# Optimization experiments

Measured on AMD Instinct MI355X. Metric: run time of the kernel, lower is better.

The kernel has to match this reference:

```python
import jax, jax.numpy as jnp
import numpy as np

B, IN, OUT = 8192, 4096, 2048  # OUT must equal 32*64 per betta/gamma sizes


def setup_inputs() -> dict:
    key = jax.random.key(0)
    kx, kw = jax.random.split(key, 2)
    X = jax.random.normal(kx, (B, IN), dtype=jnp.float32)
    # xavier-uniform-like init for W
    limit = float(np.sqrt(6.0 / (IN + OUT)))
    W = jax.random.uniform(kw, (IN, OUT), minval=-limit, maxval=limit, dtype=jnp.float32)
    absmean = jnp.abs(W).mean(axis=0)
    alpha = jnp.abs(W).mean()          # scalar, >= 0
    betta = absmean[:32]               # (32,), >= 0
    gamma = absmean[32:96]             # (64,), >= 0
    return {"X": X, "W": W, "alpha": alpha, "betta": betta, "gamma": gamma}


def reference(X, W, alpha, betta, gamma):
    # module applies relu_ to alpha/betta/gamma data before the functional call
    alpha = jax.nn.relu(alpha)
    betta = jax.nn.relu(betta)
    gamma = jax.nn.relu(gamma)
    X_bin = jnp.sign(X)                # (B, IN)
    W_bin = jnp.sign(W)                # (IN, OUT)
    # scale[i*64+j] = alpha * betta[i] * gamma[j] -> (OUT,)
    scale = (alpha * jnp.outer(betta, gamma)).reshape(-1)
    return (X_bin @ W_bin) * scale     # (B, OUT)
```

## Files before the change

### kernel.cpp

```cpp
#include <hip/hip_runtime.h>


#define M_DIM 8192
#define K_DIM 4096
#define N_DIM 2048
#define KB    (K_DIM / 2)

typedef int i32x4 __attribute__((ext_vector_type(4)));
typedef int i32x8 __attribute__((ext_vector_type(8)));
typedef float f32x16 __attribute__((ext_vector_type(16)));

__device__ __forceinline__ unsigned int nib4(float x) {
  unsigned int s = (__float_as_uint(x) >> 28) & 0x8u;
  return x == 0.0f ? 0u : (0x2u | s);
}

__device__ __forceinline__ void gload_lds16(const void* g, void* lds) {
  __builtin_amdgcn_global_load_lds(
      (const __attribute__((address_space(1))) unsigned int*)g,
      (__attribute__((address_space(3))) unsigned int*)lds, 16, 0, 0);
}

__global__ void binX4_kernel(const float* __restrict__ X,
                             unsigned int* __restrict__ Xq, int n16) {
  int stride = gridDim.x * blockDim.x;
  for (int i = blockIdx.x * blockDim.x + threadIdx.x; i < n16; i += stride) {
    size_t base = (size_t)i * 16;
    unsigned int lo = 0, hi = 0;
#pragma unroll
    for (int j = 0; j < 2; ++j) {
      float4 v0 = *(const float4*)&X[base + j * 8];
      float4 v1 = *(const float4*)&X[base + j * 8 + 4];
      unsigned int p = 0;
      p |= nib4(v0.x) << 0;  p |= nib4(v0.y) << 4;
      p |= nib4(v0.z) << 8;  p |= nib4(v0.w) << 12;
      p |= nib4(v1.x) << 16; p |= nib4(v1.y) << 20;
      p |= nib4(v1.z) << 24; p |= nib4(v1.w) << 28;
      if (j == 0) lo = p; else hi = p;
    }
    uint2 r; r.x = lo; r.y = hi;
    *(uint2*)&Xq[(size_t)i * 2] = r;
  }
}

__global__ void binW4_kernel(const float* __restrict__ W,
                             unsigned short* __restrict__ Wq) {
  __shared__ float tile[32][33];
  const int n0 = blockIdx.x * 32;
  const int k0 = blockIdx.y * 32;
  const int t = threadIdx.x;
  const int tc = t & 31;
  const int tr = t >> 5;
#pragma unroll
  for (int i = 0; i < 32; i += 8)
    tile[tr + i][tc] = W[(size_t)(k0 + tr + i) * N_DIM + n0 + tc];
  __syncthreads();
  const int r = t >> 3;
  const int c = t & 7;
  unsigned int b0 = nib4(tile[c * 4 + 0][r]) | (nib4(tile[c * 4 + 1][r]) << 4);
  unsigned int b1 = nib4(tile[c * 4 + 2][r]) | (nib4(tile[c * 4 + 3][r]) << 4);
  Wq[(size_t)(n0 + r) * (KB / 2) + (k0 >> 2) + c] = (unsigned short)(b0 | (b1 << 8));
}

__global__ __launch_bounds__(256) void gemm_fp4_kernel(
    const unsigned char* __restrict__ Aq,
    const unsigned char* __restrict__ Bq,
    const float* __restrict__ alpha,
    const float* __restrict__ betta,
    const float* __restrict__ gamma,
    float* __restrict__ C) {
  __shared__ __align__(16) unsigned char sA[128 * 128];
  __shared__ __align__(16) unsigned char sB[128 * 128];

  const int t = threadIdx.x;
  const int lane = t & 63;
  const int l31 = lane & 31;
  const int lhi = lane >> 5;
  const int w = t >> 6;
  const int wr = w >> 1, wc = w & 1;

  const int bid = blockIdx.x;
  const int bm = bid >> 4;
  const int bn = bid & 15;
  const int row0 = bm * 128;
  const int col0 = bn * 128;

  f32x16 acc[2][2];
#pragma unroll
  for (int m = 0; m < 2; ++m)
#pragma unroll
    for (int n = 0; n < 2; ++n)
#pragma unroll
      for (int r = 0; r < 16; ++r) acc[m][n][r] = 0.f;

  for (int ktb = 0; ktb < KB; ktb += 128) {
#pragma unroll
    for (int j = 0; j < 4; ++j) {
      int c = j * 256 + t;
      int r = c >> 3;
      int gg = (c & 7) ^ (r & 7);
      gload_lds16(&Aq[(size_t)(row0 + r) * KB + ktb + gg * 16], &sA[c * 16]);
      gload_lds16(&Bq[(size_t)(col0 + r) * KB + ktb + gg * 16], &sB[c * 16]);
    }
    __syncthreads();

#pragma unroll
    for (int kk = 0; kk < 4; ++kk) {
      const int g = kk * 2 + lhi;
      i32x8 av[2], bv[2];
#pragma unroll
      for (int fm = 0; fm < 2; ++fm) {
        const int rr = wr * 64 + fm * 32 + l31;
        i32x4 v = *(const i32x4*)&sA[rr * 128 + ((g ^ (rr & 7)) * 16)];
        av[fm][0] = v[0]; av[fm][1] = v[1]; av[fm][2] = v[2]; av[fm][3] = v[3];
        av[fm][4] = 0; av[fm][5] = 0; av[fm][6] = 0; av[fm][7] = 0;
      }
#pragma unroll
      for (int fn = 0; fn < 2; ++fn) {
        const int rr = wc * 64 + fn * 32 + l31;
        i32x4 v = *(const i32x4*)&sB[rr * 128 + ((g ^ (rr & 7)) * 16)];
        bv[fn][0] = v[0]; bv[fn][1] = v[1]; bv[fn][2] = v[2]; bv[fn][3] = v[3];
        bv[fn][4] = 0; bv[fn][5] = 0; bv[fn][6] = 0; bv[fn][7] = 0;
      }
#pragma unroll
      for (int fm = 0; fm < 2; ++fm)
#pragma unroll
        for (int fn = 0; fn < 2; ++fn)
          acc[fm][fn] = __builtin_amdgcn_mfma_scale_f32_32x32x64_f8f6f4(
              av[fm], bv[fn], acc[fm][fn], 4, 4,
              0, 0x7F7F7F7F, 0, 0x7F7F7F7F);
    }
    __syncthreads();
  }

  const float ra = fmaxf(alpha[0], 0.0f);
#pragma unroll
  for (int fn = 0; fn < 2; ++fn) {
    const int col = col0 + wc * 64 + fn * 32 + l31;
    const float sc = ra * fmaxf(betta[col >> 6], 0.0f) * fmaxf(gamma[col & 63], 0.0f);
#pragma unroll
    for (int fm = 0; fm < 2; ++fm) {
      const int rbase = row0 + wr * 64 + fm * 32 + 4 * lhi;
#pragma unroll
      for (int r = 0; r < 16; ++r) {
        const int row = rbase + (r & 3) + 8 * (r >> 2);
        C[(size_t)row * N_DIM + col] = acc[fm][fn][r] * sc;
      }
    }
  }
}

extern "C" void kernel_launch(void* const* d_in, const int* in_sizes, int n_in,
                              void* d_out, int out_size, void* d_ws, size_t ws_size,
                              hipStream_t stream) {
  const float* X = (const float*)d_in[0];
  const float* W = (const float*)d_in[1];
  const float* alpha = (const float*)d_in[2];
  const float* betta = (const float*)d_in[3];
  const float* gamma = (const float*)d_in[4];
  float* out = (float*)d_out;

  unsigned char* Xq = (unsigned char*)d_ws;
  unsigned char* Wq = Xq + (size_t)M_DIM * KB;

  binX4_kernel<<<2048, 256, 0, stream>>>(X, (unsigned int*)Xq,
                                         (M_DIM * K_DIM) / 16);
  binW4_kernel<<<dim3(N_DIM / 32, K_DIM / 32), 256, 0, stream>>>(
      W, (unsigned short*)Wq);
  gemm_fp4_kernel<<<(M_DIM / 128) * (N_DIM / 128), 256, 0, stream>>>(
      Xq, Wq, alpha, betta, gamma, out);
}
```

Before: 80.00 us.

## Double-buffer LDS with 256x256 tiles, 512 threads and block swizzle

```diff
diff --git a/kernel.cpp b/kernel.cpp
--- a/kernel.cpp
+++ b/kernel.cpp
@@ -5,6 +5,7 @@
 #define K_DIM 4096
 #define N_DIM 2048
 #define KB    (K_DIM / 2)
+#define NT    (K_DIM / 256)
 
 typedef int i32x4 __attribute__((ext_vector_type(4)));
 typedef int i32x8 __attribute__((ext_vector_type(8)));
@@ -19,6 +20,13 @@
   __builtin_amdgcn_global_load_lds(
       (const __attribute__((address_space(1))) unsigned int*)g,
       (__attribute__((address_space(3))) unsigned int*)lds, 16, 0, 0);
+}
+
+__device__ __forceinline__ i32x8 pad8(i32x4 v) {
+  i32x8 r;
+  r[0] = v[0]; r[1] = v[1]; r[2] = v[2]; r[3] = v[3];
+  r[4] = 0; r[5] = 0; r[6] = 0; r[7] = 0;
+  return r;
 }
 
 __global__ void binX4_kernel(const float* __restrict__ X,
@@ -62,75 +70,100 @@
   Wq[(size_t)(n0 + r) * (KB / 2) + (k0 >> 2) + c] = (unsigned short)(b0 | (b1 << 8));
 }
 
-__global__ __launch_bounds__(256) void gemm_fp4_kernel(
+__device__ __forceinline__ void stage_tile(const unsigned char* __restrict__ src,
+                                           unsigned char* lds, int t) {
+#pragma unroll
+  for (int p = 0; p < 4; ++p) {
+    int c = p * 512 + t;
+    int r = c >> 3;
+    int gg = (c & 7) ^ (r & 7);
+    gload_lds16(src + (size_t)r * KB + gg * 16, lds + c * 16);
+  }
+}
+
+__global__ __launch_bounds__(512, 2) void gemm_fp4_kernel(
     const unsigned char* __restrict__ Aq,
     const unsigned char* __restrict__ Bq,
     const float* __restrict__ alpha,
     const float* __restrict__ betta,
     const float* __restrict__ gamma,
     float* __restrict__ C) {
-  __shared__ __align__(16) unsigned char sA[128 * 128];
-  __shared__ __align__(16) unsigned char sB[128 * 128];
+  __shared__ __align__(16) unsigned char smem[131072];
 
   const int t = threadIdx.x;
   const int lane = t & 63;
   const int l31 = lane & 31;
   const int lhi = lane >> 5;
   const int w = t >> 6;
-  const int wr = w >> 1, wc = w & 1;
+  const int wr = w >> 2;
+  const int wc = w & 3;
 
   const int bid = blockIdx.x;
-  const int bm = bid >> 4;
-  const int bn = bid & 15;
-  const int row0 = bm * 128;
-  const int col0 = bn * 128;
-
-  f32x16 acc[2][2];
-#pragma unroll
-  for (int m = 0; m < 2; ++m)
-#pragma unroll
-    for (int n = 0; n < 2; ++n)
-#pragma unroll
-      for (int r = 0; r < 16; ++r) acc[m][n][r] = 0.f;
-
-  for (int ktb = 0; ktb < KB; ktb += 128) {
-#pragma unroll
-    for (int j = 0; j < 4; ++j) {
-      int c = j * 256 + t;
-      int r = c >> 3;
-      int gg = (c & 7) ^ (r & 7);
-      gload_lds16(&Aq[(size_t)(row0 + r) * KB + ktb + gg * 16], &sA[c * 16]);
-      gload_lds16(&Bq[(size_t)(col0 + r) * KB + ktb + gg * 16], &sB[c * 16]);
-    }
-    __syncthreads();
+  const int swz = (bid & 7) * 32 + (bid >> 3);
+  const int bn = swz >> 5;
+  const int bm = swz & 31;
+  const int row0 = bm * 256;
+  const int col0 = bn * 256;
+
+  const unsigned char* Asrc = Aq + (size_t)row0 * KB;
+  const unsigned char* Bsrc = Bq + (size_t)col0 * KB;
+
+  f32x16 acc[4][2];
+#pragma unroll
+  for (int fm = 0; fm < 4; ++fm)
+#pragma unroll
+    for (int fn = 0; fn < 2; ++fn)
+#pragma unroll
+      for (int r = 0; r < 16; ++r) acc[fm][fn][r] = 0.f;
+
+  stage_tile(Asrc, &smem[0], t);
+  stage_tile(Bsrc, &smem[32768], t);
+  asm volatile("s_waitcnt vmcnt(0)" ::: "memory");
+  __builtin_amdgcn_s_barrier();
+
+  for (int kt = 0; kt < NT; ++kt) {
+    const int cur = kt & 1;
+    const unsigned char* pA = &smem[cur * 65536];
+    const unsigned char* pB = pA + 32768;
+    const int nktb = (kt + 1) * 128;
 
 #pragma unroll
     for (int kk = 0; kk < 4; ++kk) {
       const int g = kk * 2 + lhi;
-      i32x8 av[2], bv[2];
-#pragma unroll
-      for (int fm = 0; fm < 2; ++fm) {
-        const int rr = wr * 64 + fm * 32 + l31;
-        i32x4 v = *(const i32x4*)&sA[rr * 128 + ((g ^ (rr & 7)) * 16)];
-        av[fm][0] = v[0]; av[fm][1] = v[1]; av[fm][2] = v[2]; av[fm][3] = v[3];
-        av[fm][4] = 0; av[fm][5] = 0; av[fm][6] = 0; av[fm][7] = 0;
+      i32x4 a4[4], b4[2];
+#pragma unroll
+      for (int fm = 0; fm < 4; ++fm) {
+        const int rr = wr * 128 + fm * 32 + l31;
+        a4[fm] = *(const i32x4*)&pA[rr * 128 + ((g ^ (rr & 7)) * 16)];
       }
 #pragma unroll
       for (int fn = 0; fn < 2; ++fn) {
         const int rr = wc * 64 + fn * 32 + l31;
-        i32x4 v = *(const i32x4*)&sB[rr * 128 + ((g ^ (rr & 7)) * 16)];
-        bv[fn][0] = v[0]; bv[fn][1] = v[1]; bv[fn][2] = v[2]; bv[fn][3] = v[3];
-        bv[fn][4] = 0; bv[fn][5] = 0; bv[fn][6] = 0; bv[fn][7] = 0;
-      }
-#pragma unroll
-      for (int fm = 0; fm < 2; ++fm)
+        b4[fn] = *(const i32x4*)&pB[rr * 128 + ((g ^ (rr & 7)) * 16)];
+      }
+      if (kk == 0 && kt + 1 < NT)
+        stage_tile(Asrc + nktb, &smem[(cur ^ 1) * 65536], t);
+      if (kk == 1 && kt + 1 < NT)
+        stage_tile(Bsrc + nktb, &smem[(cur ^ 1) * 65536 + 32768], t);
+
+      __builtin_amdgcn_s_barrier();
+      asm volatile("s_waitcnt lgkmcnt(0)" ::: "memory");
+      __builtin_amdgcn_sched_barrier(0);
+      __builtin_amdgcn_s_setprio(1);
+#pragma unroll
+      for (int fm = 0; fm < 4; ++fm) {
+        i32x8 av = pad8(a4[fm]);
 #pragma unroll
         for (int fn = 0; fn < 2; ++fn)
           acc[fm][fn] = __builtin_amdgcn_mfma_scale_f32_32x32x64_f8f6f4(
-              av[fm], bv[fn], acc[fm][fn], 4, 4,
+              av, pad8(b4[fn]), acc[fm][fn], 4, 4,
               0, 0x7F7F7F7F, 0, 0x7F7F7F7F);
+      }
+      __builtin_amdgcn_s_setprio(0);
+      if (kk < 3) __builtin_amdgcn_s_barrier();
     }
-    __syncthreads();
+    asm volatile("s_waitcnt vmcnt(0)" ::: "memory");
+    __builtin_amdgcn_s_barrier();
   }
 
   const float ra = fmaxf(alpha[0], 0.0f);
@@ -139,8 +172,8 @@
     const int col = col0 + wc * 64 + fn * 32 + l31;
     const float sc = ra * fmaxf(betta[col >> 6], 0.0f) * fmaxf(gamma[col & 63], 0.0f);
 #pragma unroll
-    for (int fm = 0; fm < 2; ++fm) {
-      const int rbase = row0 + wr * 64 + fm * 32 + 4 * lhi;
+    for (int fm = 0; fm < 4; ++fm) {
+      const int rbase = row0 + wr * 128 + fm * 32 + 4 * lhi;
 #pragma unroll
       for (int r = 0; r < 16; ++r) {
         const int row = rbase + (r & 3) + 8 * (r >> 2);
@@ -167,6 +200,6 @@
                                          (M_DIM * K_DIM) / 16);
   binW4_kernel<<<dim3(N_DIM / 32, K_DIM / 32), 256, 0, stream>>>(
       W, (unsigned short*)Wq);
-  gemm_fp4_kernel<<<(M_DIM / 128) * (N_DIM / 128), 256, 0, stream>>>(
+  gemm_fp4_kernel<<<(M_DIM / 256) * (N_DIM / 256), 512, 0, stream>>>(
       Xq, Wq, alpha, betta, gamma, out);
 }
```

After: 75.51 us. 5.6% less time.
